# Kernel optimization log

Measured on AMD Instinct MI355X. Metric: run time of the kernel, lower is better.

Reference implementation:

```python
import jax, jax.numpy as jnp
import numpy as np

EMBED_DIM = 1024
NUM_HEADS = 16
HEAD_DIM = EMBED_DIM // NUM_HEADS


def setup_inputs() -> dict:
    key = jax.random.key(0)
    k_x, k_wq, k_bq, k_wo, k_bo = jax.random.split(key, 5)
    B, S, E = 4, 2048, EMBED_DIM
    lim_qkv = 1.0 / np.sqrt(E)
    lim_out = 1.0 / np.sqrt(E)
    return {
        "x": jax.random.normal(k_x, (B, S, E), dtype=jnp.float32),
        # nn.Linear stores weight [out, in]; we keep [in, out] for x @ W
        "w_qkv": jax.random.uniform(k_wq, (E, 3 * E), minval=-lim_qkv, maxval=lim_qkv, dtype=jnp.float32),
        "b_qkv": jax.random.uniform(k_bq, (3 * E,), minval=-lim_qkv, maxval=lim_qkv, dtype=jnp.float32),
        "w_out": jax.random.uniform(k_wo, (E, E), minval=-lim_out, maxval=lim_out, dtype=jnp.float32),
        "b_out": jax.random.uniform(k_bo, (E,), minval=-lim_out, maxval=lim_out, dtype=jnp.float32),
    }


def reference(x, w_qkv, b_qkv, w_out, b_out):
    B, S, E = x.shape
    H, D = NUM_HEADS, HEAD_DIM
    qkv = x @ w_qkv + b_qkv                       # [B, S, 3E]
    qkv = qkv.reshape(B, S, H, 3 * D)
    q, k, v = jnp.split(qkv, 3, axis=-1)          # each [B, S, H, D]
    scale = 1.0 / np.sqrt(D).astype(np.float32)
    scores = jnp.einsum("bshd,bthd->bhst", q, k) * scale  # [B, H, S, S]
    attn = jax.nn.softmax(scores, axis=-1)
    out = jnp.einsum("bhst,bthd->bshd", attn, v)  # [B, S, H, D]
    out = out.reshape(B, S, E)
    return out @ w_out + b_out
```

## Files before the change

### kernel.cpp

```cpp
#include <hip/hip_runtime.h>
#include <hip/hip_bf16.h>


typedef short bf16x8 __attribute__((ext_vector_type(8)));
typedef unsigned short u16x8 __attribute__((ext_vector_type(8)));
typedef short s16x4 __attribute__((ext_vector_type(4)));
typedef float f32x4 __attribute__((ext_vector_type(4)));

#define QSCALE 0.18033688011112042f

__device__ inline short f2bf(float f) {
    unsigned int u = __builtin_bit_cast(unsigned int, f);
    u += 0x7fffu + ((u >> 16) & 1u);
    return (short)(u >> 16);
}

__device__ inline unsigned int pack2bf(float a, float b) {
#if __has_builtin(__builtin_amdgcn_cvt_pk_bf16_f32)
    typedef __bf16 bf2 __attribute__((ext_vector_type(2)));
    bf2 v = __builtin_amdgcn_cvt_pk_bf16_f32(a, b);
    return __builtin_bit_cast(unsigned int, v);
#else
    return (unsigned int)(unsigned short)f2bf(a) |
           ((unsigned int)(unsigned short)f2bf(b) << 16);
#endif
}

__device__ inline float fast_exp2(float x) {
#if __has_builtin(__builtin_amdgcn_exp2f)
    return __builtin_amdgcn_exp2f(x);
#else
    float r;
    asm("v_exp_f32 %0, %1" : "=v"(r) : "v"(x));
    return r;
#endif
}

__device__ inline float fast_rcp(float x) {
#if __has_builtin(__builtin_amdgcn_rcpf)
    return __builtin_amdgcn_rcpf(x);
#else
    float r;
    asm("v_rcp_f32 %0, %1" : "=v"(r) : "v"(x));
    return r;
#endif
}

__device__ inline void gload_lds16(const short* g, short* l) {
    __builtin_amdgcn_global_load_lds(
        (const __attribute__((address_space(1))) unsigned int*)g,
        (__attribute__((address_space(3))) unsigned int*)l, 16, 0, 0);
}


__global__ __launch_bounds__(256) void cvt_bf16_kernel(const float* __restrict__ in,
                                                       short* __restrict__ out) {
    int i = blockIdx.x * 256 + threadIdx.x;
    const float4 a = *(const float4*)(in + (size_t)i * 8);
    const float4 b = *(const float4*)(in + (size_t)i * 8 + 4);
    unsigned int o0 = pack2bf(a.x, a.y), o1 = pack2bf(a.z, a.w);
    unsigned int o2 = pack2bf(b.x, b.y), o3 = pack2bf(b.z, b.w);
    uint4 o = {o0, o1, o2, o3};
    *(uint4*)(out + (size_t)i * 8) = o;
}

__global__ __launch_bounds__(256) void transpose_cvt_kernel(const float* __restrict__ in,
                                                            short* __restrict__ out,
                                                            int K, int N) {
    __shared__ float tile[32][33];
    int tx = threadIdx.x & 31, ty = threadIdx.x >> 5;
    int nt = blockIdx.x * 32, kt = blockIdx.y * 32;
    for (int i = 0; i < 4; ++i)
        tile[ty + i * 8][tx] = in[(size_t)(kt + ty + i * 8) * N + nt + tx];
    __syncthreads();
    for (int i = 0; i < 4; ++i)
        out[(size_t)(nt + ty + i * 8) * K + kt + tx] = f2bf(tile[tx][ty + i * 8]);
}

__global__ __launch_bounds__(256, 2) void gemm_qkv_kernel(
        const short* __restrict__ A, const short* __restrict__ Bt,
        const float* __restrict__ bias,
        short* __restrict__ Qg, short* __restrict__ Kg, short* __restrict__ Vtg) {
    __shared__ short As[128 * 64];
    __shared__ short Bs[128 * 64];
    const int t = threadIdx.x;
    const int w = t >> 6, lane = t & 63, r = lane & 15, q4 = lane >> 4;
    const int n0 = blockIdx.x * 128, m0 = blockIdx.y * 128;
    const int wm = (w & 1) * 64, wn = (w >> 1) * 64;

    f32x4 acc[4][4];
    for (int i = 0; i < 4; ++i)
        for (int j = 0; j < 4; ++j)
            acc[i][j] = (f32x4){0.f, 0.f, 0.f, 0.f};

    for (int kk = 0; kk < 1024; kk += 64) {
        for (int ii = 0; ii < 4; ++ii) {
            const int p = t + 256 * ii;
            const int row = p >> 3;
            const int gg = (p & 7) ^ (row & 7);
            gload_lds16(A + (size_t)(m0 + row) * 1024 + kk + gg * 8, &As[p * 8]);
            gload_lds16(Bt + (size_t)(n0 + row) * 1024 + kk + gg * 8, &Bs[p * 8]);
        }
        __syncthreads();
        for (int ko = 0; ko < 2; ++ko) {
            bf16x8 af[4], bfr[4];
            for (int i = 0; i < 4; ++i) {
                const int R = wm + i * 16 + r;
                af[i] = *(const bf16x8*)(&As[R * 64 + (((ko * 4 + q4) ^ (R & 7)) * 8)]);
            }
            for (int j = 0; j < 4; ++j) {
                const int R = wn + j * 16 + r;
                bfr[j] = *(const bf16x8*)(&Bs[R * 64 + (((ko * 4 + q4) ^ (R & 7)) * 8)]);
            }
            for (int i = 0; i < 4; ++i)
                for (int j = 0; j < 4; ++j)
                    acc[i][j] = __builtin_amdgcn_mfma_f32_16x16x32_bf16(af[i], bfr[j], acc[i][j], 0, 0, 0);
        }
        __syncthreads();
    }

    for (int i = 0; i < 4; ++i) {
        for (int j = 0; j < 4; ++j) {
            const int gn = n0 + wn + j * 16 + r;
            const int h = gn / 192;
            const int rr = gn - h * 192;
            const float bv = bias[gn];
            for (int g = 0; g < 4; ++g) {
                const int gm = m0 + wm + i * 16 + q4 * 4 + g;
                const int bb = gm >> 11;
                const int s2 = gm & 2047;
                float v = acc[i][j][g] + bv;
                const size_t bh = (size_t)(bb * 16 + h);
                if (rr < 64) {
                    Qg[(bh * 2048 + s2) * 64 + rr] = f2bf(v * QSCALE);
                } else if (rr < 128) {
                    Kg[(bh * 2048 + s2) * 64 + (rr - 64)] = f2bf(v);
                } else {
                    Vtg[(bh * 64 + (rr - 128)) * 2048 + s2] = f2bf(v);
                }
            }
        }
    }
}

__global__ __launch_bounds__(256, 4) void attn_kernel(
        const short* __restrict__ Qg, const short* __restrict__ Kg,
        const short* __restrict__ Vtg, short* __restrict__ Og) {
    __shared__ short Ks[64 * 64];
    __shared__ short Vs[64 * 64];
    __shared__ short Ps[128 * 64];
    const int t = threadIdx.x;
    const int w = t >> 6, lane = t & 63, r = lane & 15, q4 = lane >> 4;
    const int blk = blockIdx.x;
    const int qt = blk & 15;
    const int h = (blk >> 4) & 15;
    const int b = blk >> 8;
    const size_t bh = (size_t)b * 16 + h;
    const short* Qb = Qg + bh * 2048 * 64;
    const short* Kb = Kg + bh * 2048 * 64;
    const short* Vb = Vtg + bh * 64 * 2048;

    const int r1 = t >> 3, g1 = (t & 7) ^ (r1 & 7);
    const int r2 = 32 + (t >> 3), g2 = (t & 7) ^ (r2 & 7);
    const short* kptr1 = Kb + r1 * 64 + g1 * 8;
    const short* kptr2 = Kb + r2 * 64 + g2 * 8;
    const short* vptr1 = Vb + (size_t)r1 * 2048 + g1 * 8;
    const short* vptr2 = Vb + (size_t)r2 * 2048 + g2 * 8;
    short* klds1 = &Ks[t * 8];
    short* klds2 = &Ks[(256 + t) * 8];
    short* vlds1 = &Vs[t * 8];
    short* vlds2 = &Vs[(256 + t) * 8];

    const int swz = r & 7;
    const int ga = (q4 ^ swz) * 8;
    const int gb = ((4 + q4) ^ swz) * 8;

    bf16x8 qf[2][2];
    for (int qs = 0; qs < 2; ++qs) {
        const int qrow = qt * 128 + w * 32 + qs * 16 + r;
        qf[qs][0] = *(const bf16x8*)(Qb + (size_t)qrow * 64 + q4 * 8);
        qf[qs][1] = *(const bf16x8*)(Qb + (size_t)qrow * 64 + 32 + q4 * 8);
    }

    bf16x8 onesf;
    for (int i = 0; i < 8; ++i) onesf[i] = (short)0x3F80;

    f32x4 o[2][4], ol[2];
    for (int qs = 0; qs < 2; ++qs) {
        ol[qs] = (f32x4){0.f, 0.f, 0.f, 0.f};
        for (int nt = 0; nt < 4; ++nt) o[qs][nt] = (f32x4){0.f, 0.f, 0.f, 0.f};
    }

    const int pbase0 = w * 2048;
    const int pwb = pbase0 + r * 64 + (q4 & 1) * 4;
    const int pgq = q4 >> 1;
    const int prb = pbase0 + r * 64;

    for (int kt = 0; kt < 32; ++kt) {
        gload_lds16(kptr1 + kt * 4096, klds1);
        gload_lds16(kptr2 + kt * 4096, klds2);
        gload_lds16(vptr1 + kt * 64, vlds1);
        gload_lds16(vptr2 + kt * 64, vlds2);
        __syncthreads();

        f32x4 st[2][4];
        for (int c = 0; c < 4; ++c) {
            const int R = (c * 16 + r) * 64;
            const bf16x8 kf0 = *(const bf16x8*)(&Ks[R + ga]);
            const bf16x8 kf1 = *(const bf16x8*)(&Ks[R + gb]);
            for (int qs = 0; qs < 2; ++qs) {
                f32x4 z = (f32x4){0.f, 0.f, 0.f, 0.f};
                z = __builtin_amdgcn_mfma_f32_16x16x32_bf16(kf0, qf[qs][0], z, 0, 0, 0);
                z = __builtin_amdgcn_mfma_f32_16x16x32_bf16(kf1, qf[qs][1], z, 0, 0, 0);
                st[qs][c] = z;
            }
        }

        for (int qs = 0; qs < 2; ++qs) {
            const int pb = pwb + qs * 1024;
            for (int c = 0; c < 4; ++c) {
                const float p0 = fast_exp2(st[qs][c][0]);
                const float p1 = fast_exp2(st[qs][c][1]);
                const float p2 = fast_exp2(st[qs][c][2]);
                const float p3 = fast_exp2(st[qs][c][3]);
                uint2 pk = {pack2bf(p0, p1), pack2bf(p2, p3)};
                *(uint2*)(&Ps[pb + (((c * 2 + pgq) ^ swz) * 8)]) = pk;
            }
        }
        asm volatile("s_waitcnt lgkmcnt(0)" ::: "memory");

        for (int ko = 0; ko < 2; ++ko) {
            const int gk = (ko == 0) ? ga : gb;
            bf16x8 pf[2];
            for (int qs = 0; qs < 2; ++qs)
                pf[qs] = *(const bf16x8*)(&Ps[prb + qs * 1024 + (((ko * 4 + q4) ^ swz) * 8)]);
            for (int qs = 0; qs < 2; ++qs)
                ol[qs] = __builtin_amdgcn_mfma_f32_16x16x32_bf16(onesf, pf[qs], ol[qs], 0, 0, 0);
            for (int nt = 0; nt < 4; ++nt) {
                const bf16x8 vf = *(const bf16x8*)(&Vs[(nt * 16 + r) * 64 + gk]);
                for (int qs = 0; qs < 2; ++qs)
                    o[qs][nt] = __builtin_amdgcn_mfma_f32_16x16x32_bf16(vf, pf[qs], o[qs][nt], 0, 0, 0);
            }
        }
        __syncthreads();
    }

    for (int qs = 0; qs < 2; ++qs) {
        const float inv = fast_rcp(ol[qs][0]);
        const int srow = qt * 128 + w * 32 + qs * 16 + r;
        const size_t base = ((size_t)(b * 2048 + srow)) * 1024 + h * 64;
        for (int nt = 0; nt < 4; ++nt) {
            uint2 pk = {pack2bf(o[qs][nt][0] * inv, o[qs][nt][1] * inv),
                        pack2bf(o[qs][nt][2] * inv, o[qs][nt][3] * inv)};
            *(uint2*)(Og + base + nt * 16 + q4 * 4) = pk;
        }
    }
}

__global__ __launch_bounds__(256, 2) void gemm_out_kernel(
        const short* __restrict__ A, const short* __restrict__ Bt,
        const float* __restrict__ bias, float* __restrict__ out) {
    __shared__ short As[128 * 64];
    __shared__ short Bs[128 * 64];
    const int t = threadIdx.x;
    const int w = t >> 6, lane = t & 63, r = lane & 15, q4 = lane >> 4;
    const int n0 = blockIdx.x * 128, m0 = blockIdx.y * 128;
    const int wm = (w & 1) * 64, wn = (w >> 1) * 64;

    f32x4 acc[4][4];
    for (int i = 0; i < 4; ++i)
        for (int j = 0; j < 4; ++j)
            acc[i][j] = (f32x4){0.f, 0.f, 0.f, 0.f};

    for (int kk = 0; kk < 1024; kk += 64) {
        for (int ii = 0; ii < 4; ++ii) {
            const int p = t + 256 * ii;
            const int row = p >> 3;
            const int gg = (p & 7) ^ (row & 7);
            gload_lds16(A + (size_t)(m0 + row) * 1024 + kk + gg * 8, &As[p * 8]);
            gload_lds16(Bt + (size_t)(n0 + row) * 1024 + kk + gg * 8, &Bs[p * 8]);
        }
        __syncthreads();
        for (int ko = 0; ko < 2; ++ko) {
            bf16x8 af[4], bfr[4];
            for (int i = 0; i < 4; ++i) {
                const int R = wm + i * 16 + r;
                af[i] = *(const bf16x8*)(&As[R * 64 + (((ko * 4 + q4) ^ (R & 7)) * 8)]);
            }
            for (int j = 0; j < 4; ++j) {
                const int R = wn + j * 16 + r;
                bfr[j] = *(const bf16x8*)(&Bs[R * 64 + (((ko * 4 + q4) ^ (R & 7)) * 8)]);
            }
            for (int i = 0; i < 4; ++i)
                for (int j = 0; j < 4; ++j)
                    acc[i][j] = __builtin_amdgcn_mfma_f32_16x16x32_bf16(af[i], bfr[j], acc[i][j], 0, 0, 0);
        }
        __syncthreads();
    }

    for (int i = 0; i < 4; ++i) {
        for (int j = 0; j < 4; ++j) {
            const int gn = n0 + wn + j * 16 + r;
            const float bv = bias[gn];
            for (int g = 0; g < 4; ++g) {
                const int gm = m0 + wm + i * 16 + q4 * 4 + g;
                out[(size_t)gm * 1024 + gn] = acc[i][j][g] + bv;
            }
        }
    }
}


extern "C" void kernel_launch(void* const* d_in, const int* in_sizes, int n_in,
                              void* d_out, int out_size, void* d_ws, size_t ws_size,
                              hipStream_t stream) {
    const float* x     = (const float*)d_in[0];
    const float* w_qkv = (const float*)d_in[1];
    const float* b_qkv = (const float*)d_in[2];
    const float* w_out = (const float*)d_in[3];
    const float* b_out = (const float*)d_in[4];
    float* out = (float*)d_out;

    char* ws = (char*)d_ws;
    short* xb    = (short*)(ws);
    short* wqkvT = (short*)(ws + 16777216);
    short* woutT = (short*)(ws + 23068672);
    short* Qg    = (short*)(ws + 25165824);
    short* Kg    = (short*)(ws + 41943040);
    short* Vtg   = (short*)(ws + 58720256);
    short* attn  = xb;

    cvt_bf16_kernel<<<4096, 256, 0, stream>>>(x, xb);
    transpose_cvt_kernel<<<dim3(96, 32), 256, 0, stream>>>(w_qkv, wqkvT, 1024, 3072);
    transpose_cvt_kernel<<<dim3(32, 32), 256, 0, stream>>>(w_out, woutT, 1024, 1024);
    gemm_qkv_kernel<<<dim3(24, 64), 256, 0, stream>>>(xb, wqkvT, b_qkv, Qg, Kg, Vtg);
    attn_kernel<<<1024, 256, 0, stream>>>(Qg, Kg, Vtg, attn);
    gemm_out_kernel<<<dim3(8, 64), 256, 0, stream>>>(attn, woutT, b_out, out);
}
```

Measured before the change: 279.6 us.

## Double-buffer V in LDS, read K directly from global, remap blocks

The attention kernel now double-buffers the V tile in LDS, prefetching the next tile while the current one is consumed, and drops the per-iteration pre-barrier. K fragments are loaded straight from global memory into registers rather than staged through LDS. The block index is permuted so that neighbouring blocks land on different heads or batches, and s_setprio raises wave priority around the MFMA sections. This is meant to hide global load latency and cut barriers, at the cost of uncached-pattern global K reads and more LDS for two V buffers.

```diff
diff --git a/kernel.cpp b/kernel.cpp
--- a/kernel.cpp
+++ b/kernel.cpp
@@ -146,12 +146,12 @@
 __global__ __launch_bounds__(256, 4) void attn_kernel(
         const short* __restrict__ Qg, const short* __restrict__ Kg,
         const short* __restrict__ Vtg, short* __restrict__ Og) {
-    __shared__ short Ks[64 * 64];
-    __shared__ short Vs[64 * 64];
+    __shared__ short Vs[2][64 * 64];
     __shared__ short Ps[128 * 64];
     const int t = threadIdx.x;
     const int w = t >> 6, lane = t & 63, r = lane & 15, q4 = lane >> 4;
-    const int blk = blockIdx.x;
+    const int blk0 = blockIdx.x;
+    const int blk = ((blk0 & 7) << 7) | (blk0 >> 3);
     const int qt = blk & 15;
     const int h = (blk >> 4) & 15;
     const int b = blk >> 8;
@@ -162,14 +162,8 @@
 
     const int r1 = t >> 3, g1 = (t & 7) ^ (r1 & 7);
     const int r2 = 32 + (t >> 3), g2 = (t & 7) ^ (r2 & 7);
-    const short* kptr1 = Kb + r1 * 64 + g1 * 8;
-    const short* kptr2 = Kb + r2 * 64 + g2 * 8;
     const short* vptr1 = Vb + (size_t)r1 * 2048 + g1 * 8;
     const short* vptr2 = Vb + (size_t)r2 * 2048 + g2 * 8;
-    short* klds1 = &Ks[t * 8];
-    short* klds2 = &Ks[(256 + t) * 8];
-    short* vlds1 = &Vs[t * 8];
-    short* vlds2 = &Vs[(256 + t) * 8];
 
     const int swz = r & 7;
     const int ga = (q4 ^ swz) * 8;
@@ -196,24 +190,34 @@
     const int pgq = q4 >> 1;
     const int prb = pbase0 + r * 64;
 
+    const short* kfb = Kb + (size_t)r * 64 + q4 * 8;
+
+    gload_lds16(vptr1, &Vs[0][t * 8]);
+    gload_lds16(vptr2, &Vs[0][(256 + t) * 8]);
+    __syncthreads();
+
+    int buf = 0;
     for (int kt = 0; kt < 32; ++kt) {
-        gload_lds16(kptr1 + kt * 4096, klds1);
-        gload_lds16(kptr2 + kt * 4096, klds2);
-        gload_lds16(vptr1 + kt * 64, vlds1);
-        gload_lds16(vptr2 + kt * 64, vlds2);
-        __syncthreads();
+        const int nb = buf ^ 1;
 
         f32x4 st[2][4];
+        __builtin_amdgcn_s_setprio(1);
         for (int c = 0; c < 4; ++c) {
-            const int R = (c * 16 + r) * 64;
-            const bf16x8 kf0 = *(const bf16x8*)(&Ks[R + ga]);
-            const bf16x8 kf1 = *(const bf16x8*)(&Ks[R + gb]);
+            const short* kp = kfb + (size_t)(kt * 64 + c * 16) * 64;
+            const bf16x8 kf0 = *(const bf16x8*)(kp);
+            const bf16x8 kf1 = *(const bf16x8*)(kp + 32);
             for (int qs = 0; qs < 2; ++qs) {
                 f32x4 z = (f32x4){0.f, 0.f, 0.f, 0.f};
                 z = __builtin_amdgcn_mfma_f32_16x16x32_bf16(kf0, qf[qs][0], z, 0, 0, 0);
                 z = __builtin_amdgcn_mfma_f32_16x16x32_bf16(kf1, qf[qs][1], z, 0, 0, 0);
                 st[qs][c] = z;
             }
+        }
+        __builtin_amdgcn_s_setprio(0);
+
+        if (kt + 1 < 32) {
+            gload_lds16(vptr1 + (kt + 1) * 64, &Vs[nb][t * 8]);
+            gload_lds16(vptr2 + (kt + 1) * 64, &Vs[nb][(256 + t) * 8]);
         }
 
         for (int qs = 0; qs < 2; ++qs) {
@@ -229,6 +233,8 @@
         }
         asm volatile("s_waitcnt lgkmcnt(0)" ::: "memory");
 
+        const short* Vl = Vs[buf];
+        __builtin_amdgcn_s_setprio(1);
         for (int ko = 0; ko < 2; ++ko) {
             const int gk = (ko == 0) ? ga : gb;
             bf16x8 pf[2];
@@ -237,12 +243,15 @@
             for (int qs = 0; qs < 2; ++qs)
                 ol[qs] = __builtin_amdgcn_mfma_f32_16x16x32_bf16(onesf, pf[qs], ol[qs], 0, 0, 0);
             for (int nt = 0; nt < 4; ++nt) {
-                const bf16x8 vf = *(const bf16x8*)(&Vs[(nt * 16 + r) * 64 + gk]);
+                const bf16x8 vf = *(const bf16x8*)(&Vl[(nt * 16 + r) * 64 + gk]);
                 for (int qs = 0; qs < 2; ++qs)
                     o[qs][nt] = __builtin_amdgcn_mfma_f32_16x16x32_bf16(vf, pf[qs], o[qs][nt], 0, 0, 0);
             }
         }
-        __syncthreads();
+        __builtin_amdgcn_s_setprio(0);
+
+        __syncthreads();
+        buf = nb;
     }
 
     for (int qs = 0; qs < 2; ++qs) {
```

Result: slower. 312.8 us (+11.9%).
